# Kernel tuning notes

Measured on AMD Instinct MI355X. Metric: run time of the kernel, lower is better.

The kernel has to match this reference:

```python
import jax, jax.numpy as jnp
import numpy as np

B, STATE_DIM, ACTION_DIM = 16384, 512, 64
HID, NQ, QED = 1024, 64, 64
EPS = 1e-5


def _layernorm(x, gamma, beta):
    mu = jnp.mean(x, axis=-1, keepdims=True)
    var = jnp.mean(jnp.square(x - mu), axis=-1, keepdims=True)
    return (x - mu) * jax.lax.rsqrt(var + EPS) * gamma + beta


def setup_inputs() -> dict:
    key = jax.random.key(0)
    ks = jax.random.split(key, 12)
    s = 0.02  # small init scale for stable activations
    return {
        "state": jax.random.normal(ks[0], (B, STATE_DIM), jnp.float32),
        "action": jax.random.normal(ks[1], (B, ACTION_DIM), jnp.float32),
        "W1": jax.random.normal(ks[2], (STATE_DIM + ACTION_DIM, HID), jnp.float32) * s,
        "b1": jax.random.normal(ks[3], (HID,), jnp.float32) * s,
        "g1": jnp.ones((HID,), jnp.float32),
        "be1": jnp.zeros((HID,), jnp.float32),
        "W2": jax.random.normal(ks[4], (HID, HID), jnp.float32) * s,
        "b2": jax.random.normal(ks[5], (HID,), jnp.float32) * s,
        "g2": jnp.ones((HID,), jnp.float32),
        "be2": jnp.zeros((HID,), jnp.float32),
        "Wq1": jax.random.normal(ks[6], (1, QED), jnp.float32) * s,
        "bq1": jax.random.normal(ks[7], (QED,), jnp.float32) * s,
        "Wq2": jax.random.normal(ks[8], (QED, QED), jnp.float32) * s,
        "bq2": jax.random.normal(ks[9], (QED,), jnp.float32) * s,
        "Wh": jax.random.normal(ks[10], (HID + QED, 1), jnp.float32) * s,
        "bh": jax.random.normal(ks[11], (1,), jnp.float32) * s,
    }


def reference(state, action, W1, b1, g1, be1, W2, b2, g2, be2,
              Wq1, bq1, Wq2, bq2, Wh, bh):
    # tau buffer: midpoints of NQ uniform bins
    tau = jnp.linspace(0.0, 1.0, NQ + 1)[:-1] + 1.0 / (2 * NQ)  # [NQ]

    # feature_net (Dropout is identity in eval)
    x = jnp.concatenate([state, action], axis=-1)               # [B, S+A]
    h = jax.nn.relu(_layernorm(x @ W1 + b1, g1, be1))           # [B, HID]
    h = jax.nn.relu(_layernorm(h @ W2 + b2, g2, be2))           # [B, HID]

    # quantile embedding: tau rows are batch-independent -> one [NQ, QED] MLP
    te = jax.nn.relu(tau[:, None] @ Wq1 + bq1) @ Wq2 + bq2      # [NQ, QED]

    # head on concat([features, tau_emb]) == split the head weight
    Wf, Wt = Wh[:HID, 0], Wh[HID:, 0]                           # [HID], [QED]
    quantiles = h @ Wf[:, None] + (te @ Wt)[None, :] + bh[0]    # [B, NQ]
    return quantiles
```

## Files before the change

kernel.cpp:

```cpp
#include <hip/hip_runtime.h>
#include <hip/hip_bf16.h>
#include <cstddef>

#define B_ROWS 16384
#define SDIM 512
#define ADIM 64
#define KDIM 576
#define KPAD1 640
#define HID 1024
#define NQ 64

#define SEG0_ITEMS (B_ROWS * (SDIM / 8))
#define SEG1_ITEMS (B_ROWS * (ADIM / 8))
#define SEG2_ITEMS (B_ROWS * ((KPAD1 - KDIM) / 8))
#define EW_ITEMS (SEG0_ITEMS + SEG1_ITEMS + SEG2_ITEMS)
#define EW_BLOCKS 2048
#define T1_BLOCKS 640
#define T2_BLOCKS 1024
#define PREP_BLOCKS (EW_BLOCKS + T1_BLOCKS + T2_BLOCKS + 1)

typedef __attribute__((ext_vector_type(8))) __bf16 bf16x8;
typedef __attribute__((ext_vector_type(4))) float f32x4;

static __device__ __forceinline__ float bf2f(unsigned short u) {
  union { unsigned int i; float f; } x; x.i = ((unsigned int)u) << 16; return x.f;
}
static __device__ __forceinline__ unsigned short f2bf(float f) {
  union { float f; unsigned int i; } x; x.f = f;
  unsigned int i = x.i + (0x7fffu + ((x.i >> 16) & 1u));
  return (unsigned short)(i >> 16);
}

static __device__ __forceinline__ void gload_lds16(const unsigned short* g, unsigned short* l) {
  __builtin_amdgcn_global_load_lds(
      (const __attribute__((address_space(1))) void*)(const void*)g,
      (__attribute__((address_space(3))) void*)(void*)l, 16, 0, 0);
}

static __device__ __forceinline__ ushort4 cvt8lo(float4 a) {
  ushort4 o; o.x = f2bf(a.x); o.y = f2bf(a.y); o.z = f2bf(a.z); o.w = f2bf(a.w);
  return o;
}

static __device__ __forceinline__ void transpose_body(
    const float* __restrict__ W, unsigned short* __restrict__ Wb,
    int Kin, int Kpad, int N, int k0, int n0, unsigned short* tile ) {
  const int tx = threadIdx.x & 31, ty = threadIdx.x >> 5;
#pragma unroll
  for (int i = 0; i < 32; i += 8) {
    const int k = k0 + ty + i;
    tile[(ty + i) * 33 + tx] = (k < Kin) ? f2bf(W[(size_t)k * N + n0 + tx]) : (unsigned short)0;
  }
  __syncthreads();
#pragma unroll
  for (int i = 0; i < 32; i += 8)
    Wb[(size_t)(n0 + ty + i) * Kpad + k0 + tx] = tile[tx * 33 + ty + i];
}

__global__ __launch_bounds__(256) void prep_k(
    const float* __restrict__ state, const float* __restrict__ action,
    const float* __restrict__ W1, const float* __restrict__ W2,
    const float* __restrict__ Wq1, const float* __restrict__ bq1,
    const float* __restrict__ Wq2, const float* __restrict__ bq2,
    const float* __restrict__ Wh, const float* __restrict__ bh,
    unsigned short* __restrict__ xb, unsigned short* __restrict__ w1b,
    unsigned short* __restrict__ w2b, float* __restrict__ qoff) {
  __shared__ unsigned short tile[32 * 33];
  const int b = blockIdx.x;
  if (b < EW_BLOCKS) {
    for (int i = b * 256 + (int)threadIdx.x; i < EW_ITEMS; i += EW_BLOCKS * 256) {
      if (i < SEG0_ITEMS) {
        const int r = i >> 6, c = (i & 63) << 3;
        const float* sp = state + (size_t)r * SDIM + c;
        float4 a = *(const float4*)sp;
        float4 bb = *(const float4*)(sp + 4);
        unsigned short* yp = xb + (size_t)r * KPAD1 + c;
        *(ushort4*)yp = cvt8lo(a);
        *(ushort4*)(yp + 4) = cvt8lo(bb);
      } else if (i < SEG0_ITEMS + SEG1_ITEMS) {
        const int j = i - SEG0_ITEMS;
        const int r = j >> 3, ca = (j & 7) << 3;
        const float* ap = action + (size_t)r * ADIM + ca;
        float4 a = *(const float4*)ap;
        float4 bb = *(const float4*)(ap + 4);
        unsigned short* yp = xb + (size_t)r * KPAD1 + SDIM + ca;
        *(ushort4*)yp = cvt8lo(a);
        *(ushort4*)(yp + 4) = cvt8lo(bb);
      } else {
        const int j = i - SEG0_ITEMS - SEG1_ITEMS;
        const int r = j >> 3, cz = (j & 7) << 3;
        unsigned short* yp = xb + (size_t)r * KPAD1 + KDIM + cz;
        ushort4 z = {0, 0, 0, 0};
        *(ushort4*)yp = z;
        *(ushort4*)(yp + 4) = z;
      }
    }
  } else if (b < EW_BLOCKS + T1_BLOCKS) {
    const int t = b - EW_BLOCKS;
    transpose_body(W1, w1b, KDIM, KPAD1, HID, (t / 32) * 32, (t % 32) * 32, tile);
  } else if (b < EW_BLOCKS + T1_BLOCKS + T2_BLOCKS) {
    const int t = b - EW_BLOCKS - T1_BLOCKS;
    transpose_body(W2, w2b, HID, HID, HID, (t / 32) * 32, (t % 32) * 32, tile);
  } else {
    const int q = threadIdx.x;
    if (q < NQ) {
      const float tau = ((float)q + 0.5f) * (1.0f / (float)NQ);
      float t1[64];
#pragma unroll
      for (int k = 0; k < 64; ++k) t1[k] = fmaxf(fmaf(tau, Wq1[k], bq1[k]), 0.f);
      float acc = bh[0];
#pragma unroll 1
      for (int j = 0; j < 64; ++j) {
        float t2 = bq2[j];
#pragma unroll
        for (int k = 0; k < 64; ++k) t2 = fmaf(t1[k], Wq2[k * 64 + j], t2);
        acc = fmaf(t2, Wh[HID + j], acc);
      }
      qoff[q] = acc;
    }
  }
}

__global__ __launch_bounds__(512, 2) void gemm8_k(
    const unsigned short* __restrict__ A, const unsigned short* __restrict__ Bt,
    const float* __restrict__ bias, unsigned short* __restrict__ C,
    int N, int K, int NT) {
  extern __shared__ unsigned short sm[];
  const int tid = threadIdx.x;
  const int w = tid >> 6, l = tid & 63;

  const int cpx = (int)gridDim.x >> 3;
  int bid = (int)blockIdx.x;
  bid = (bid & 7) * cpx + (bid >> 3);
  const int nb = N >> 8;
  const int m0 = (bid / nb) << 8, n0 = (bid % nb) << 8;

  const int srow0 = w * 8 + (l >> 3);
  const int sce = ((((l & 7) << 4) ^ ((srow0 & 4) << 3)) >> 1);

  const int aB = (w >> 2) * 16384;
  const int bB = 65536 + ((w & 3) >> 1) * 16384;
  const int lr = (l & 15) << 7;
  const int bRow = (w & 1) << 13;
  const int cSw = (((l >> 4) << 4) ^ ((l & 4) << 3));

  f32x4 acc[8][4] = {};
  bf16x8 ra[2][4], rb[2][4];

#define AF(d, mi, kk) (*(const bf16x8*)(sm + ((aB + (d)*32768 + (mi)*2048 + lr + cSw + ((kk) << 6)) >> 1)))
#define BFR(d, ni, kk) (*(const bf16x8*)(sm + ((bB + (d)*32768 + bRow + (ni)*2048 + lr + cSw + ((kk) << 6)) >> 1)))
#define STGA(d, h, kt) do { \
    const unsigned short* g_ = A + (size_t)(m0 + (h)*128 + srow0) * K + (kt) + sce; \
    unsigned short* l_ = sm + (((d)*32768 + (h)*16384 + w*1024) >> 1); \
    gload_lds16(g_, l_); gload_lds16(g_ + (size_t)64 * K, l_ + 4096); } while (0)
#define STGB(d, h, kt) do { \
    const unsigned short* g_ = Bt + (size_t)(n0 + (h)*128 + srow0) * K + (kt) + sce; \
    unsigned short* l_ = sm + ((65536 + (d)*32768 + (h)*16384 + w*1024) >> 1); \
    gload_lds16(g_, l_); gload_lds16(g_ + (size_t)64 * K, l_ + 4096); } while (0)
#define RDA(d, base) do { _Pragma("unroll") for (int kk = 0; kk < 2; ++kk) \
    _Pragma("unroll") for (int mi = 0; mi < 4; ++mi) ra[kk][mi] = AF(d, (base) + mi, kk); } while (0)
#define RDB(d, base) do { _Pragma("unroll") for (int kk = 0; kk < 2; ++kk) \
    _Pragma("unroll") for (int ni = 0; ni < 2; ++ni) rb[kk][(base) + ni] = BFR(d, (base) + ni, kk); } while (0)
#define MQ(MO, NO) do { _Pragma("unroll") for (int kk = 0; kk < 2; ++kk) \
    _Pragma("unroll") for (int mi = 0; mi < 4; ++mi) \
    _Pragma("unroll") for (int ni = 0; ni < 2; ++ni) \
      acc[(MO) + mi][(NO) + ni] = __builtin_amdgcn_mfma_f32_16x16x32_bf16( \
          ra[kk][mi], rb[kk][(NO) + ni], acc[(MO) + mi][(NO) + ni], 0, 0, 0); } while (0)
#define BAR() __builtin_amdgcn_s_barrier()
#define WAITLGKM() asm volatile("s_waitcnt lgkmcnt(0)" ::: "memory")
#define WAITLGKM8() asm volatile("s_waitcnt lgkmcnt(8)" ::: "memory")
#define WAITVM(n) asm volatile("s_waitcnt vmcnt(" #n ")" ::: "memory")

  STGA(0, 0, 0); STGA(0, 1, 0); STGB(0, 0, 0); STGB(0, 1, 0);
  STGB(1, 0, 64); STGB(1, 1, 64);
  WAITVM(4); BAR();

  for (int t = 0; t < NT; t += 2) {
    const int kt1 = (t + 1) << 6;
    const int kt2 = ((t + 2 < NT) ? (t + 2) : (NT - 1)) << 6;
    const int kt3 = ((t + 3 < NT) ? (t + 3) : (NT - 1)) << 6;
    RDA(0, 0); RDB(0, 0); STGA(1, 0, kt1);
    WAITLGKM8();
    BAR(); WAITLGKM();
    __builtin_amdgcn_s_setprio(1); MQ(0, 0); __builtin_amdgcn_s_setprio(0);
    BAR();
    RDB(0, 2); STGA(1, 1, kt1);
    BAR(); WAITLGKM();
    __builtin_amdgcn_s_setprio(1); MQ(0, 2); __builtin_amdgcn_s_setprio(0);
    BAR();
    RDA(0, 4); STGB(0, 0, kt2);
    BAR(); WAITLGKM();
    __builtin_amdgcn_s_setprio(1); MQ(4, 2); __builtin_amdgcn_s_setprio(0);
    BAR();
    STGB(0, 1, kt2);
    BAR();
    __builtin_amdgcn_s_setprio(1); MQ(4, 0); __builtin_amdgcn_s_setprio(0);
    WAITVM(4); BAR();
    RDA(1, 0); RDB(1, 0); STGA(0, 0, kt2);
    WAITLGKM8();
    BAR(); WAITLGKM();
    __builtin_amdgcn_s_setprio(1); MQ(0, 0); __builtin_amdgcn_s_setprio(0);
    BAR();
    RDB(1, 2); STGA(0, 1, kt2);
    BAR(); WAITLGKM();
    __builtin_amdgcn_s_setprio(1); MQ(0, 2); __builtin_amdgcn_s_setprio(0);
    BAR();
    RDA(1, 4); STGB(1, 0, kt3);
    BAR(); WAITLGKM();
    __builtin_amdgcn_s_setprio(1); MQ(4, 2); __builtin_amdgcn_s_setprio(0);
    BAR();
    STGB(1, 1, kt3);
    BAR();
    __builtin_amdgcn_s_setprio(1); MQ(4, 0); __builtin_amdgcn_s_setprio(0);
    WAITVM(4); BAR();
  }

  WAITVM(0);
  const int wr = (w >> 2) << 7, wc = (w & 3) << 6;
#pragma unroll
  for (int mi = 0; mi < 8; ++mi) {
    const int row = m0 + wr + mi * 16 + ((l >> 4) << 2);
#pragma unroll
    for (int ni = 0; ni < 4; ++ni) {
      const int col = n0 + wc + ni * 16 + (l & 15);
      const float bc = bias[col];
#pragma unroll
      for (int r = 0; r < 4; ++r)
        C[(size_t)(row + r) * N + col] = f2bf(acc[mi][ni][r] + bc);
    }
  }
#undef AF
#undef BFR
#undef STGA
#undef STGB
#undef RDA
#undef RDB
#undef MQ
#undef BAR
#undef WAITLGKM
#undef WAITLGKM8
#undef WAITVM
}

__global__ __launch_bounds__(256) void ln_relu_k(
    const unsigned short* __restrict__ X, const float* __restrict__ g,
    const float* __restrict__ be, unsigned short* __restrict__ Y) {
  const int w = threadIdx.x >> 6, l = threadIdx.x & 63;
  const size_t row = (size_t)blockIdx.x * 4 + w;
  const unsigned short* xr = X + row * HID;
  float v[16];
  float sum = 0.f, ss = 0.f;
#pragma unroll
  for (int c = 0; c < 4; ++c) {
    ushort4 u = *(const ushort4*)(xr + (c * 64 + l) * 4);
    float a0 = bf2f(u.x), a1 = bf2f(u.y), a2 = bf2f(u.z), a3 = bf2f(u.w);
    v[c * 4 + 0] = a0; v[c * 4 + 1] = a1; v[c * 4 + 2] = a2; v[c * 4 + 3] = a3;
    sum += a0 + a1 + a2 + a3;
    ss += a0 * a0 + a1 * a1 + a2 * a2 + a3 * a3;
  }
#pragma unroll
  for (int o = 32; o > 0; o >>= 1) {
    sum += __shfl_xor(sum, o, 64);
    ss  += __shfl_xor(ss, o, 64);
  }
  const float mu = sum * (1.f / HID);
  const float rs = rsqrtf(ss * (1.f / HID) - mu * mu + 1e-5f);
  unsigned short* yr = Y + row * HID;
#pragma unroll
  for (int c = 0; c < 4; ++c) {
    const int col = (c * 64 + l) * 4;
    float4 gg = *(const float4*)(g + col);
    float4 bb = *(const float4*)(be + col);
    ushort4 o4;
    o4.x = f2bf(fmaxf((v[c * 4 + 0] - mu) * rs * gg.x + bb.x, 0.f));
    o4.y = f2bf(fmaxf((v[c * 4 + 1] - mu) * rs * gg.y + bb.y, 0.f));
    o4.z = f2bf(fmaxf((v[c * 4 + 2] - mu) * rs * gg.z + bb.z, 0.f));
    o4.w = f2bf(fmaxf((v[c * 4 + 3] - mu) * rs * gg.w + bb.w, 0.f));
    *(ushort4*)(yr + col) = o4;
  }
}

__global__ __launch_bounds__(256) void ln_final_k(
    const unsigned short* __restrict__ X, const float* __restrict__ g,
    const float* __restrict__ be, const float* __restrict__ Wh,
    const float* __restrict__ qoff, float* __restrict__ out) {
  const int w = threadIdx.x >> 6, l = threadIdx.x & 63;
  const size_t row = (size_t)blockIdx.x * 4 + w;
  const unsigned short* xr = X + row * HID;
  float v[16];
  float sum = 0.f, ss = 0.f;
#pragma unroll
  for (int c = 0; c < 4; ++c) {
    ushort4 u = *(const ushort4*)(xr + (c * 64 + l) * 4);
    float a0 = bf2f(u.x), a1 = bf2f(u.y), a2 = bf2f(u.z), a3 = bf2f(u.w);
    v[c * 4 + 0] = a0; v[c * 4 + 1] = a1; v[c * 4 + 2] = a2; v[c * 4 + 3] = a3;
    sum += a0 + a1 + a2 + a3;
    ss += a0 * a0 + a1 * a1 + a2 * a2 + a3 * a3;
  }
#pragma unroll
  for (int o = 32; o > 0; o >>= 1) {
    sum += __shfl_xor(sum, o, 64);
    ss  += __shfl_xor(ss, o, 64);
  }
  const float mu = sum * (1.f / HID);
  const float rs = rsqrtf(ss * (1.f / HID) - mu * mu + 1e-5f);
  float dot = 0.f;
#pragma unroll
  for (int c = 0; c < 4; ++c) {
    const int col = (c * 64 + l) * 4;
    float4 gg = *(const float4*)(g + col);
    float4 bb = *(const float4*)(be + col);
    float4 wf = *(const float4*)(Wh + col);
    dot += fmaxf((v[c * 4 + 0] - mu) * rs * gg.x + bb.x, 0.f) * wf.x;
    dot += fmaxf((v[c * 4 + 1] - mu) * rs * gg.y + bb.y, 0.f) * wf.y;
    dot += fmaxf((v[c * 4 + 2] - mu) * rs * gg.z + bb.z, 0.f) * wf.z;
    dot += fmaxf((v[c * 4 + 3] - mu) * rs * gg.w + bb.w, 0.f) * wf.w;
  }
#pragma unroll
  for (int o = 32; o > 0; o >>= 1) dot += __shfl_xor(dot, o, 64);
  out[row * NQ + l] = dot + qoff[l];
}

extern "C" void kernel_launch(void* const* d_in, const int* in_sizes, int n_in,
                              void* d_out, int out_size, void* d_ws, size_t ws_size,
                              hipStream_t stream) {
  const float* state  = (const float*)d_in[0];
  const float* action = (const float*)d_in[1];
  const float* W1  = (const float*)d_in[2];
  const float* b1  = (const float*)d_in[3];
  const float* g1  = (const float*)d_in[4];
  const float* be1 = (const float*)d_in[5];
  const float* W2  = (const float*)d_in[6];
  const float* b2  = (const float*)d_in[7];
  const float* g2  = (const float*)d_in[8];
  const float* be2 = (const float*)d_in[9];
  const float* Wq1 = (const float*)d_in[10];
  const float* bq1 = (const float*)d_in[11];
  const float* Wq2 = (const float*)d_in[12];
  const float* bq2 = (const float*)d_in[13];
  const float* Wh  = (const float*)d_in[14];
  const float* bh  = (const float*)d_in[15];
  float* out = (float*)d_out;

  char* ws = (char*)d_ws;
  size_t off = 0;
  float* qoff = (float*)(ws + off); off += 256;
  unsigned short* xb  = (unsigned short*)(ws + off); off += (size_t)B_ROWS * KPAD1 * 2;
  unsigned short* w1b = (unsigned short*)(ws + off); off += (size_t)HID * KPAD1 * 2;
  unsigned short* w2b = (unsigned short*)(ws + off); off += (size_t)HID * HID * 2;
  unsigned short* h1b = (unsigned short*)(ws + off); off += (size_t)B_ROWS * HID * 2;
  unsigned short* tb  = (unsigned short*)(ws + off);

  hipFuncSetAttribute((const void*)gemm8_k, hipFuncAttributeMaxDynamicSharedMemorySize, 131072);

  prep_k<<<PREP_BLOCKS, 256, 0, stream>>>(state, action, W1, W2, Wq1, bq1, Wq2, bq2,
                                          Wh, bh, xb, w1b, w2b, qoff);

  gemm8_k<<<(B_ROWS / 256) * (HID / 256), 512, 131072, stream>>>(xb, w1b, b1, tb, HID, KPAD1, KPAD1 / 64);
  ln_relu_k<<<B_ROWS / 4, 256, 0, stream>>>(tb, g1, be1, h1b);
  gemm8_k<<<(B_ROWS / 256) * (HID / 256), 512, 131072, stream>>>(h1b, w2b, b2, tb, HID, HID, HID / 64);
  ln_final_k<<<B_ROWS / 4, 256, 0, stream>>>(tb, g2, be2, Wh, qoff, out);
}
```

Before: 121.1 us.

## Fuse first LayerNorm+ReLU into second GEMM prologue via epilogue row statistics

The first GEMM's epilogue now accumulates per-row sum and sum-of-squares and adds them into a stats buffer with atomics. The second GEMM loads A tiles through registers, applies LayerNorm, gamma/beta and ReLU on the fly, and writes the normalized bf16 values into LDS, so the standalone ln_relu kernel and its full read/write of the hidden activation go away. In exchange the A path loses the async global-to-LDS loads and adds VALU work and register pressure inside the pipelined main loop, and statistics are taken from fp32 values before bf16 rounding. A memset is added for the stats buffer.

```diff
diff --git a/kernel.cpp b/kernel.cpp
--- a/kernel.cpp
+++ b/kernel.cpp
@@ -44,7 +44,7 @@
 
 static __device__ __forceinline__ void transpose_body(
     const float* __restrict__ W, unsigned short* __restrict__ Wb,
-    int Kin, int Kpad, int N, int k0, int n0, unsigned short* tile ) {
+    int Kin, int Kpad, int N, int k0, int n0, unsigned short* tile) {
   const int tx = threadIdx.x & 31, ty = threadIdx.x >> 5;
 #pragma unroll
   for (int i = 0; i < 32; i += 8) {
@@ -121,10 +121,28 @@
   }
 }
 
+static __device__ __forceinline__ void ln_wr8(
+    unsigned short* dst, uint4 u, float mu, float rs, const float* gb) {
+  uint4 ov;
+  unsigned int* op = (unsigned int*)&ov;
+  const unsigned int* ip = (const unsigned int*)&u;
+#pragma unroll
+  for (int i = 0; i < 4; ++i) {
+    float x0 = bf2f((unsigned short)(ip[i] & 0xffffu));
+    float x1 = bf2f((unsigned short)(ip[i] >> 16));
+    float y0 = fmaxf((x0 - mu) * rs * gb[2 * i] + gb[8 + 2 * i], 0.f);
+    float y1 = fmaxf((x1 - mu) * rs * gb[2 * i + 1] + gb[8 + 2 * i + 1], 0.f);
+    op[i] = (unsigned int)f2bf(y0) | ((unsigned int)f2bf(y1) << 16);
+  }
+  *(uint4*)dst = ov;
+}
+
+template <bool FUSED>
 __global__ __launch_bounds__(512, 2) void gemm8_k(
     const unsigned short* __restrict__ A, const unsigned short* __restrict__ Bt,
     const float* __restrict__ bias, unsigned short* __restrict__ C,
-    int N, int K, int NT) {
+    float* __restrict__ stats, const float* __restrict__ gLn,
+    const float* __restrict__ beLn, int N, int K, int NT) {
   extern __shared__ unsigned short sm[];
   const int tid = threadIdx.x;
   const int w = tid >> 6, l = tid & 63;
@@ -146,6 +164,10 @@
 
   f32x4 acc[8][4] = {};
   bf16x8 ra[2][4], rb[2][4];
+
+  float mu4[4], rs4[4];
+  uint4 rA[2], rB[2];
+  float gbA[16], gbB[16];
 
 #define AF(d, mi, kk) (*(const bf16x8*)(sm + ((aB + (d)*32768 + (mi)*2048 + lr + cSw + ((kk) << 6)) >> 1)))
 #define BFR(d, ni, kk) (*(const bf16x8*)(sm + ((bB + (d)*32768 + bRow + (ni)*2048 + lr + cSw + ((kk) << 6)) >> 1)))
@@ -157,6 +179,17 @@
     const unsigned short* g_ = Bt + (size_t)(n0 + (h)*128 + srow0) * K + (kt) + sce; \
     unsigned short* l_ = sm + ((65536 + (d)*32768 + (h)*16384 + w*1024) >> 1); \
     gload_lds16(g_, l_); gload_lds16(g_ + (size_t)64 * K, l_ + 4096); } while (0)
+#define ALD(regs, h, kt) do { \
+    const unsigned short* g_ = A + (size_t)(m0 + (h)*128 + srow0) * K + (kt) + sce; \
+    regs[0] = *(const uint4*)g_; regs[1] = *(const uint4*)(g_ + (size_t)64 * K); } while (0)
+#define GBLD(dst, kt) do { \
+    const float* gp_ = gLn + (kt) + sce; const float* bp_ = beLn + (kt) + sce; \
+    *(float4*)&dst[0] = *(const float4*)gp_; *(float4*)&dst[4] = *(const float4*)(gp_ + 4); \
+    *(float4*)&dst[8] = *(const float4*)bp_; *(float4*)&dst[12] = *(const float4*)(bp_ + 4); } while (0)
+#define AWR(d, h, regs, gb) do { \
+    unsigned short* l_ = sm + (((d)*32768 + (h)*16384 + w*1024 + l*16) >> 1); \
+    ln_wr8(l_, regs[0], mu4[(h)*2 + 0], rs4[(h)*2 + 0], gb); \
+    ln_wr8(l_ + 4096, regs[1], mu4[(h)*2 + 1], rs4[(h)*2 + 1], gb); } while (0)
 #define RDA(d, base) do { _Pragma("unroll") for (int kk = 0; kk < 2; ++kk) \
     _Pragma("unroll") for (int mi = 0; mi < 4; ++mi) ra[kk][mi] = AF(d, (base) + mi, kk); } while (0)
 #define RDB(d, base) do { _Pragma("unroll") for (int kk = 0; kk < 2; ++kk) \
@@ -170,69 +203,130 @@
 #define WAITLGKM() asm volatile("s_waitcnt lgkmcnt(0)" ::: "memory")
 #define WAITLGKM8() asm volatile("s_waitcnt lgkmcnt(8)" ::: "memory")
 #define WAITVM(n) asm volatile("s_waitcnt vmcnt(" #n ")" ::: "memory")
-
-  STGA(0, 0, 0); STGA(0, 1, 0); STGB(0, 0, 0); STGB(0, 1, 0);
-  STGB(1, 0, 64); STGB(1, 1, 64);
-  WAITVM(4); BAR();
+#define PRIO1() __builtin_amdgcn_s_setprio(1)
+#define PRIO0() __builtin_amdgcn_s_setprio(0)
+
+  if (!FUSED) {
+    STGA(0, 0, 0); STGA(0, 1, 0); STGB(0, 0, 0); STGB(0, 1, 0);
+    STGB(1, 0, 64); STGB(1, 1, 64);
+    WAITVM(4); BAR();
+  } else {
+#pragma unroll
+    for (int h = 0; h < 2; ++h)
+#pragma unroll
+      for (int rr = 0; rr < 2; ++rr) {
+        const int row = m0 + h * 128 + srow0 + rr * 64;
+        const float s1 = stats[row * 2], s2 = stats[row * 2 + 1];
+        const float m = s1 * (1.0f / HID);
+        mu4[h * 2 + rr] = m;
+        rs4[h * 2 + rr] = rsqrtf(s2 * (1.0f / HID) - m * m + 1e-5f);
+      }
+    ALD(rA, 0, 0); GBLD(gbA, 0); ALD(rB, 1, 0);
+    STGB(0, 0, 0); STGB(0, 1, 0);
+    AWR(0, 0, rA, gbA);
+    AWR(0, 1, rB, gbA);
+    ALD(rA, 0, 64); ALD(rB, 1, 64); GBLD(gbA, 64);
+    STGB(1, 0, 64); STGB(1, 1, 64);
+    WAITVM(12);
+    WAITLGKM();
+    BAR();
+  }
 
   for (int t = 0; t < NT; t += 2) {
     const int kt1 = (t + 1) << 6;
     const int kt2 = ((t + 2 < NT) ? (t + 2) : (NT - 1)) << 6;
     const int kt3 = ((t + 3 < NT) ? (t + 3) : (NT - 1)) << 6;
-    RDA(0, 0); RDB(0, 0); STGA(1, 0, kt1);
+    if (!FUSED) { RDA(0, 0); RDB(0, 0); STGA(1, 0, kt1); }
+    else        { AWR(1, 0, rA, gbA); RDA(0, 0); RDB(0, 0); }
     WAITLGKM8();
     BAR(); WAITLGKM();
-    __builtin_amdgcn_s_setprio(1); MQ(0, 0); __builtin_amdgcn_s_setprio(0);
-    BAR();
-    RDB(0, 2); STGA(1, 1, kt1);
-    BAR(); WAITLGKM();
-    __builtin_amdgcn_s_setprio(1); MQ(0, 2); __builtin_amdgcn_s_setprio(0);
-    BAR();
+    PRIO1(); MQ(0, 0); PRIO0();
+    BAR();
+    if (!FUSED) { RDB(0, 2); STGA(1, 1, kt1); }
+    else        { AWR(1, 1, rB, gbA); RDB(0, 2); }
+    BAR(); WAITLGKM();
+    PRIO1(); MQ(0, 2); PRIO0();
+    BAR();
+    if (FUSED) { ALD(rA, 0, kt2); GBLD(gbB, kt2); }
     RDA(0, 4); STGB(0, 0, kt2);
     BAR(); WAITLGKM();
-    __builtin_amdgcn_s_setprio(1); MQ(4, 2); __builtin_amdgcn_s_setprio(0);
-    BAR();
+    PRIO1(); MQ(4, 2); PRIO0();
+    BAR();
+    if (FUSED) { ALD(rB, 1, kt2); }
     STGB(0, 1, kt2);
     BAR();
-    __builtin_amdgcn_s_setprio(1); MQ(4, 0); __builtin_amdgcn_s_setprio(0);
-    WAITVM(4); BAR();
-    RDA(1, 0); RDB(1, 0); STGA(0, 0, kt2);
+    PRIO1(); MQ(4, 0); PRIO0();
+    if (!FUSED) { WAITVM(4); } else { WAITVM(12); }
+    BAR();
+    if (!FUSED) { RDA(1, 0); RDB(1, 0); STGA(0, 0, kt2); }
+    else        { AWR(0, 0, rA, gbB); RDA(1, 0); RDB(1, 0); }
     WAITLGKM8();
     BAR(); WAITLGKM();
-    __builtin_amdgcn_s_setprio(1); MQ(0, 0); __builtin_amdgcn_s_setprio(0);
-    BAR();
-    RDB(1, 2); STGA(0, 1, kt2);
-    BAR(); WAITLGKM();
-    __builtin_amdgcn_s_setprio(1); MQ(0, 2); __builtin_amdgcn_s_setprio(0);
-    BAR();
+    PRIO1(); MQ(0, 0); PRIO0();
+    BAR();
+    if (!FUSED) { RDB(1, 2); STGA(0, 1, kt2); }
+    else        { AWR(0, 1, rB, gbB); RDB(1, 2); }
+    BAR(); WAITLGKM();
+    PRIO1(); MQ(0, 2); PRIO0();
+    BAR();
+    if (FUSED) { ALD(rA, 0, kt3); GBLD(gbA, kt3); }
     RDA(1, 4); STGB(1, 0, kt3);
     BAR(); WAITLGKM();
-    __builtin_amdgcn_s_setprio(1); MQ(4, 2); __builtin_amdgcn_s_setprio(0);
-    BAR();
+    PRIO1(); MQ(4, 2); PRIO0();
+    BAR();
+    if (FUSED) { ALD(rB, 1, kt3); }
     STGB(1, 1, kt3);
     BAR();
-    __builtin_amdgcn_s_setprio(1); MQ(4, 0); __builtin_amdgcn_s_setprio(0);
-    WAITVM(4); BAR();
+    PRIO1(); MQ(4, 0); PRIO0();
+    if (!FUSED) { WAITVM(4); } else { WAITVM(12); }
+    BAR();
   }
 
   WAITVM(0);
   const int wr = (w >> 2) << 7, wc = (w & 3) << 6;
+  float s1s[8][4], s2s[8][4];
 #pragma unroll
   for (int mi = 0; mi < 8; ++mi) {
     const int row = m0 + wr + mi * 16 + ((l >> 4) << 2);
+#pragma unroll
+    for (int r = 0; r < 4; ++r) { s1s[mi][r] = 0.f; s2s[mi][r] = 0.f; }
 #pragma unroll
     for (int ni = 0; ni < 4; ++ni) {
       const int col = n0 + wc + ni * 16 + (l & 15);
       const float bc = bias[col];
 #pragma unroll
-      for (int r = 0; r < 4; ++r)
-        C[(size_t)(row + r) * N + col] = f2bf(acc[mi][ni][r] + bc);
+      for (int r = 0; r < 4; ++r) {
+        const float x = acc[mi][ni][r] + bc;
+        C[(size_t)(row + r) * N + col] = f2bf(x);
+        if (!FUSED) { s1s[mi][r] += x; s2s[mi][r] += x * x; }
+      }
     }
+  }
+  if (!FUSED) {
+#pragma unroll
+    for (int mi = 0; mi < 8; ++mi)
+#pragma unroll
+      for (int r = 0; r < 4; ++r) {
+        float s1 = s1s[mi][r], s2 = s2s[mi][r];
+#pragma unroll
+        for (int o = 1; o < 16; o <<= 1) {
+          s1 += __shfl_xor(s1, o, 64);
+          s2 += __shfl_xor(s2, o, 64);
+        }
+        if ((l & 15) == 0) {
+          const int row = m0 + wr + mi * 16 + ((l >> 4) << 2) + r;
+          atomicAdd(&stats[row * 2], s1);
+          atomicAdd(&stats[row * 2 + 1], s2);
+        }
+      }
   }
 #undef AF
 #undef BFR
 #undef STGA
 #undef STGB
+#undef ALD
+#undef GBLD
+#undef AWR
 #undef RDA
 #undef RDB
 #undef MQ
@@ -240,44 +334,6 @@
 #undef WAITLGKM
 #undef WAITLGKM8
 #undef WAITVM
-}
-
-__global__ __launch_bounds__(256) void ln_relu_k(
-    const unsigned short* __restrict__ X, const float* __restrict__ g,
-    const float* __restrict__ be, unsigned short* __restrict__ Y) {
-  const int w = threadIdx.x >> 6, l = threadIdx.x & 63;
-  const size_t row = (size_t)blockIdx.x * 4 + w;
-  const unsigned short* xr = X + row * HID;
-  float v[16];
-  float sum = 0.f, ss = 0.f;
-#pragma unroll
-  for (int c = 0; c < 4; ++c) {
-    ushort4 u = *(const ushort4*)(xr + (c * 64 + l) * 4);
-    float a0 = bf2f(u.x), a1 = bf2f(u.y), a2 = bf2f(u.z), a3 = bf2f(u.w);
-    v[c * 4 + 0] = a0; v[c * 4 + 1] = a1; v[c * 4 + 2] = a2; v[c * 4 + 3] = a3;
-    sum += a0 + a1 + a2 + a3;
-    ss += a0 * a0 + a1 * a1 + a2 * a2 + a3 * a3;
-  }
-#pragma unroll
-  for (int o = 32; o > 0; o >>= 1) {
-    sum += __shfl_xor(sum, o, 64);
-    ss  += __shfl_xor(ss, o, 64);
-  }
-  const float mu = sum * (1.f / HID);
-  const float rs = rsqrtf(ss * (1.f / HID) - mu * mu + 1e-5f);
-  unsigned short* yr = Y + row * HID;
-#pragma unroll
-  for (int c = 0; c < 4; ++c) {
-    const int col = (c * 64 + l) * 4;
-    float4 gg = *(const float4*)(g + col);
-    float4 bb = *(const float4*)(be + col);
-    ushort4 o4;
-    o4.x = f2bf(fmaxf((v[c * 4 + 0] - mu) * rs * gg.x + bb.x, 0.f));
-    o4.y = f2bf(fmaxf((v[c * 4 + 1] - mu) * rs * gg.y + bb.y, 0.f));
-    o4.z = f2bf(fmaxf((v[c * 4 + 2] - mu) * rs * gg.z + bb.z, 0.f));
-    o4.w = f2bf(fmaxf((v[c * 4 + 3] - mu) * rs * gg.w + bb.w, 0.f));
-    *(ushort4*)(yr + col) = o4;
-  }
 }
 
 __global__ __launch_bounds__(256) void ln_final_k(
@@ -344,20 +400,24 @@
 
   char* ws = (char*)d_ws;
   size_t off = 0;
-  float* qoff = (float*)(ws + off); off += 256;
+  float* qoff  = (float*)(ws + off); off += 256;
+  float* stats = (float*)(ws + off); off += (size_t)B_ROWS * 2 * 4;
   unsigned short* xb  = (unsigned short*)(ws + off); off += (size_t)B_ROWS * KPAD1 * 2;
   unsigned short* w1b = (unsigned short*)(ws + off); off += (size_t)HID * KPAD1 * 2;
   unsigned short* w2b = (unsigned short*)(ws + off); off += (size_t)HID * HID * 2;
-  unsigned short* h1b = (unsigned short*)(ws + off); off += (size_t)B_ROWS * HID * 2;
-  unsigned short* tb  = (unsigned short*)(ws + off);
-
-  hipFuncSetAttribute((const void*)gemm8_k, hipFuncAttributeMaxDynamicSharedMemorySize, 131072);
-
+  unsigned short* tb  = (unsigned short*)(ws + off); off += (size_t)B_ROWS * HID * 2;
+  unsigned short* tb2 = (unsigned short*)(ws + off);
+
+  (void)hipFuncSetAttribute((const void*)gemm8_k<false>, hipFuncAttributeMaxDynamicSharedMemorySize, 131072);
+  (void)hipFuncSetAttribute((const void*)gemm8_k<true>, hipFuncAttributeMaxDynamicSharedMemorySize, 131072);
+
+  (void)hipMemsetAsync(stats, 0, (size_t)B_ROWS * 2 * 4, stream);
   prep_k<<<PREP_BLOCKS, 256, 0, stream>>>(state, action, W1, W2, Wq1, bq1, Wq2, bq2,
                                           Wh, bh, xb, w1b, w2b, qoff);
 
-  gemm8_k<<<(B_ROWS / 256) * (HID / 256), 512, 131072, stream>>>(xb, w1b, b1, tb, HID, KPAD1, KPAD1 / 64);
-  ln_relu_k<<<B_ROWS / 4, 256, 0, stream>>>(tb, g1, be1, h1b);
-  gemm8_k<<<(B_ROWS / 256) * (HID / 256), 512, 131072, stream>>>(h1b, w2b, b2, tb, HID, HID, HID / 64);
-  ln_final_k<<<B_ROWS / 4, 256, 0, stream>>>(tb, g2, be2, Wh, qoff, out);
-}
+  gemm8_k<false><<<(B_ROWS / 256) * (HID / 256), 512, 131072, stream>>>(
+      xb, w1b, b1, tb, stats, nullptr, nullptr, HID, KPAD1, KPAD1 / 64);
+  gemm8_k<true><<<(B_ROWS / 256) * (HID / 256), 512, 131072, stream>>>(
+      tb, w2b, b2, tb2, stats, g1, be1, HID, HID, HID / 64);
+  ln_final_k<<<B_ROWS / 4, 256, 0, stream>>>(tb2, g2, be2, Wh, qoff, out);
+}
```

Measured after the change: 159.5 us. +31.7%, slower.
